# Optimization experiments

Measured on AMD Instinct MI355X. Metric: run time of the kernel, lower is better.

The kernel has to match this reference:

```python
import jax, jax.numpy as jnp
import numpy as np

N_TOKENS = 16384
DIM = 4096
NUM_EXPERTS = 128
TOP_K = 8


def setup_inputs() -> dict:
    key = jax.random.key(0)
    k1, k2 = jax.random.split(key)
    x = jax.random.normal(k1, (N_TOKENS, DIM), dtype=jnp.float32)
    gate_w = jax.random.normal(k2, (NUM_EXPERTS, DIM), dtype=jnp.float32) * (DIM ** -0.5)
    return {"x": x, "gate_w": gate_w, "experts_per_token": TOP_K, "num_experts": NUM_EXPERTS}


def reference(x, gate_w, experts_per_token, num_experts):
    # gate: x @ W^T -> (N, E) logits
    scores = jnp.einsum('nd,ed->ne', x, gate_w)
    # softmax in fp32, cast back to input dtype
    probs = jax.nn.softmax(scores.astype(jnp.float32), axis=-1).astype(x.dtype)
    # stable descending argsort (argsort of negated probs, stable)
    sorted_indices = jnp.argsort(-probs, axis=1, stable=True)
    selected_experts = sorted_indices[:, :experts_per_token]            # (N, k)
    top_scores = jnp.take_along_axis(probs, selected_experts, axis=1)   # (N, k)
    # norm_topk_prob=True: renormalize selected weights to sum to 1
    denom = jnp.clip(top_scores.sum(axis=-1, keepdims=True), 1e-8, None)
    top_scores = top_scores / denom
    flat_experts = selected_experts.reshape(-1)                         # (N*k,)
    num_tokens_per_expert = jnp.bincount(flat_experts, length=num_experts)
    # stable sort token-slots by expert id for expert grouping
    perm = jnp.argsort(flat_experts, stable=True)                       # (N*k,)
    top_scores_sorted = top_scores.reshape(-1)[perm]
    token_indices = perm // experts_per_token
    return top_scores_sorted, token_indices, num_tokens_per_expert
```

## Files before the change

### kernel.cpp

```cpp
#include <hip/hip_runtime.h>
#include <math.h>

typedef _Float16 f16;
typedef f16 f16x8 __attribute__((ext_vector_type(8)));
typedef float f32x4 __attribute__((ext_vector_type(4)));

#define NT    16384
#define DIM   4096
#define NEXP  128
#define TOPK  8
#define NFLAT (NT * TOPK)
#define BT    32
#define NBLK  (NT / BT)
#define BK    64
#define NSTEP (DIM / BK)

#define COUNTS_OFF 0
#define SEL_OFF    1024
#define WGT_OFF    (SEL_OFF + NFLAT * 4)
#define BH_OFF     (WGT_OFF + NFLAT * 4)
#define BO_OFF     (BH_OFF + NEXP * NBLK * 4)
#define WPK_OFF    (BO_OFF + NEXP * NBLK * 4)

#define G1P __attribute__((address_space(1)))
#define L3P __attribute__((address_space(3)))

__device__ __forceinline__ void gload_lds16(const void* g, void* l) {
    __builtin_amdgcn_global_load_lds((const G1P unsigned int*)g,
                                     (L3P unsigned int*)l, 16, 0, 0);
}

__device__ __forceinline__ void split2(float v, f16& h, f16& m) {
    h = (f16)v;
    m = (f16)((v - (float)h) * 2048.0f);
}

__global__ __launch_bounds__(256)
void wsplit_kernel(const float* __restrict__ gw, char* __restrict__ wpk) {
    const int t = blockIdx.x * 256 + threadIdx.x;
    const int l = t & 63, kkc = (t >> 6) & 1, w = (t >> 7) & 7, st = t >> 10;
    const int e = w * 16 + (l & 15);
    const int k0 = st * 64 + kkc * 32 + (l >> 4) * 8;
    float4 a = *(const float4*)&gw[e * 4096 + k0];
    float4 b = *(const float4*)&gw[e * 4096 + k0 + 4];
    union { f16 f[8]; uint4 u; } ph, pm;
    split2(a.x * 64.f, ph.f[0], pm.f[0]); split2(a.y * 64.f, ph.f[1], pm.f[1]);
    split2(a.z * 64.f, ph.f[2], pm.f[2]); split2(a.w * 64.f, ph.f[3], pm.f[3]);
    split2(b.x * 64.f, ph.f[4], pm.f[4]); split2(b.y * 64.f, ph.f[5], pm.f[5]);
    split2(b.z * 64.f, ph.f[6], pm.f[6]); split2(b.w * 64.f, ph.f[7], pm.f[7]);
    const size_t base = ((size_t)(st * 8 + w) * 4 + kkc) * 1024 + l * 16;
    *(uint4*)(wpk + base)        = ph.u;
    *(uint4*)(wpk + base + 2048) = pm.u;
}

__global__ __launch_bounds__(512, 4)
void fused_kernel(const float* __restrict__ x, const char* __restrict__ wpk,
                  float* __restrict__ wgt, int* __restrict__ sel,
                  int* __restrict__ counts, int* __restrict__ bh) {
    __shared__ __align__(16) char smem[81920];
    char* WB = smem + 16384;

    const int tid  = threadIdx.x;
    const int tok0 = blockIdx.x * BT;
    const int lane = tid & 63, w = tid >> 6;
    const int fr = lane & 15, hi = lane >> 4;
    const int srow = tid >> 4;
    const int skq  = (tid & 15) * 4;
    const int xi = srow >> 4, xfr = srow & 15;
    const int xkk = skq >> 5, xhi = (skq >> 3) & 3, xo = skq & 7;
    const int slot = xhi * 16 + xfr;
    const int xwb = ((xi * 2 + xkk) * 64 + (slot ^ (xhi << 1))) * 16 + xo * 2;
    const int lxs = (lane ^ ((lane >> 4) << 1)) * 16;

    f32x4 acc0[2], acc1[2];
#pragma unroll
    for (int i = 0; i < 2; ++i) {
        acc0[i] = (f32x4){0.f, 0.f, 0.f, 0.f};
        acc1[i] = (f32x4){0.f, 0.f, 0.f, 0.f};
    }

    const size_t xrow = (size_t)(tok0 + srow) * DIM;

#define X_PREF(RA, SI) RA = *(const float4*)&x[xrow + (size_t)(SI) * BK + skq];
#define W_PREF(SI, B) { \
    const char* wsrc = wpk + ((size_t)(SI) * 8 + w) * 4096 + lane * 16; \
    char* wdst = WB + (B) * 32768 + w * 4096; \
    gload_lds16(wsrc,        wdst); \
    gload_lds16(wsrc + 1024, wdst + 1024); \
    gload_lds16(wsrc + 2048, wdst + 2048); \
    gload_lds16(wsrc + 3072, wdst + 3072); }
#define STAGE(CUR, RA) { \
    union { f16 f[4]; uint2 u; } ph, pm; \
    split2(RA.x, ph.f[0], pm.f[0]); split2(RA.y, ph.f[1], pm.f[1]); \
    split2(RA.z, ph.f[2], pm.f[2]); split2(RA.w, ph.f[3], pm.f[3]); \
    *(uint2*)(smem + (CUR) * 4096 + xwb) = ph.u; \
    *(uint2*)(smem + 8192 + (CUR) * 4096 + xwb) = pm.u; }
#define COMPUTE(CUR) { \
    _Pragma("unroll") \
    for (int kk = 0; kk < 2; ++kk) { \
        f16x8 ah[2], am[2]; \
        _Pragma("unroll") \
        for (int i = 0; i < 2; ++i) { \
            const int xb = (CUR) * 4096 + (i * 2 + kk) * 1024 + lxs; \
            ah[i] = *(const f16x8*)(smem + xb); \
            am[i] = *(const f16x8*)(smem + 8192 + xb); \
        } \
        const int wb = (CUR) * 32768 + w * 4096 + kk * 1024 + lane * 16; \
        f16x8 bhf = *(const f16x8*)(WB + wb); \
        f16x8 bmf = *(const f16x8*)(WB + wb + 2048); \
        _Pragma("unroll") \
        for (int i = 0; i < 2; ++i) { \
            acc0[i] = __builtin_amdgcn_mfma_f32_16x16x32_f16(ah[i], bhf, acc0[i], 0, 0, 0); \
            acc1[i] = __builtin_amdgcn_mfma_f32_16x16x32_f16(ah[i], bmf, acc1[i], 0, 0, 0); \
            acc1[i] = __builtin_amdgcn_mfma_f32_16x16x32_f16(am[i], bhf, acc1[i], 0, 0, 0); \
        } \
    } }
#define STEP(CUR, RA, PX, PW, SI, VMSTR) { \
    STAGE(CUR, RA); \
    asm volatile("s_waitcnt lgkmcnt(0)" ::: "memory"); \
    __builtin_amdgcn_s_barrier(); \
    if (PX) { X_PREF(RA, (SI) + 2); } \
    if (PW) { W_PREF((SI) + 1, (CUR) ^ 1); } \
    asm volatile("s_waitcnt vmcnt(" VMSTR ")" ::: "memory"); \
    __builtin_amdgcn_sched_barrier(0); \
    __builtin_amdgcn_s_setprio(1); \
    COMPUTE(CUR); \
    __builtin_amdgcn_s_setprio(0); }

    float4 ra0, ra1;
    X_PREF(ra0, 0);
    X_PREF(ra1, 1);
    W_PREF(0, 0);

    for (int st = 0; st < 62; st += 2) {
        STEP(0, ra0, 1, 1, st, "5");
        STEP(1, ra1, 1, 1, st + 1, "5");
    }
    STEP(0, ra0, 0, 1, 62, "4");
    STEP(1, ra1, 0, 0, 63, "0");

    __syncthreads();

    float* S = (float*)smem;
    int*   h = (int*)(smem + 18432);
#pragma unroll
    for (int i = 0; i < 2; ++i)
#pragma unroll
        for (int q = 0; q < 4; ++q) {
            int t = i * 16 + hi * 4 + q;
            int e = w * 16 + fr;
            S[t * 132 + e] = (acc0[i][q] + acc1[i][q] * (1.0f / 2048.0f)) * (1.0f / 64.0f);
        }
    if (tid < NEXP) h[tid] = 0;
    __syncthreads();

    if (tid < BT) {
        float bs[8]; int bi[8];
#pragma unroll
        for (int r = 0; r < 8; ++r) { bs[r] = -3.0e38f; bi[r] = 0; }
        for (int e = 0; e < NEXP; ++e) {
            float s = S[tid * 132 + e];
            if (s > bs[7]) {
                int pos = 7;
#pragma unroll
                for (int q = 6; q >= 0; q--) pos = (s > bs[q]) ? q : pos;
#pragma unroll
                for (int q = 7; q >= 1; q--) {
                    bool sh = (q > pos);
                    bs[q] = sh ? bs[q - 1] : bs[q];
                    bi[q] = sh ? bi[q - 1] : bi[q];
                }
#pragma unroll
                for (int q = 0; q < 8; q++)
                    if (q == pos) { bs[q] = s; bi[q] = e; }
            }
        }
        float m = bs[0], sum = 0.f, ex[8];
#pragma unroll
        for (int r = 0; r < 8; ++r) { ex[r] = expf(bs[r] - m); sum += ex[r]; }
        float inv = 1.f / fmaxf(sum, 1e-8f);
        const int tok = tok0 + tid;
#pragma unroll
        for (int r = 0; r < 8; ++r) {
            wgt[tok * TOPK + r] = ex[r] * inv;
            sel[tok * TOPK + r] = bi[r];
            atomicAdd(&h[bi[r]], 1);
        }
    }
    __syncthreads();
    if (tid < NEXP) {
        int c = h[tid];
        bh[tid * NBLK + blockIdx.x] = c;
        if (c) atomicAdd(&counts[tid], c);
    }
}

__global__ void scan_kernel(const int* __restrict__ bh, const int* __restrict__ counts,
                            int* __restrict__ bo, float* __restrict__ out) {
    const int e = blockIdx.x, tid = threadIdx.x;
    __shared__ int pre[NEXP];
    __shared__ int wsum[8];
    if (tid < NEXP) pre[tid] = counts[tid];
    __syncthreads();
#pragma unroll
    for (int d = 1; d < NEXP; d <<= 1) {
        int o = (tid < NEXP && tid >= d) ? pre[tid - d] : 0;
        __syncthreads();
        if (tid < NEXP) pre[tid] += o;
        __syncthreads();
    }
    const int gb = (e == 0) ? 0 : pre[e - 1];
    if (tid == 0) out[2 * NFLAT + e] = (float)counts[e];

    const int lane = tid & 63, wid = tid >> 6;
    int v = bh[e * NBLK + tid];
    int sc = v;
#pragma unroll
    for (int d = 1; d < 64; d <<= 1) {
        int o = __shfl_up(sc, d);
        sc += (lane >= d) ? o : 0;
    }
    if (lane == 63) wsum[wid] = sc;
    __syncthreads();
    int add = 0;
#pragma unroll
    for (int ww = 0; ww < 8; ww++) add += (ww < wid) ? wsum[ww] : 0;
    bo[e * NBLK + tid] = gb + sc - v + add;
}

__global__ void scatter_kernel(const int* __restrict__ sel, const float* __restrict__ wgt,
                               const int* __restrict__ bo, float* __restrict__ out) {
    const int tid = threadIdx.x, b = blockIdx.x;
    const int i = b * 256 + tid;
    const int e = sel[i];
    const int lane = tid & 63, wid = tid >> 6;
    unsigned long long m = ~0ull;
#pragma unroll
    for (int bit = 0; bit < 7; bit++) {
        unsigned long long bal = __ballot((e >> bit) & 1);
        m &= ((e >> bit) & 1) ? bal : ~bal;
    }
    unsigned long long lower = (lane == 0) ? 0ull : (~0ull >> (64 - lane));
    int wrank = __popcll(m & lower);

    __shared__ int wh_[4][NEXP];
    ((int*)wh_)[tid] = 0; ((int*)wh_)[tid + 256] = 0;
    __syncthreads();
    if (wrank == 0) wh_[wid][e] = __popcll(m);
    __syncthreads();
    int off = 0;
#pragma unroll
    for (int ww = 0; ww < 4; ww++) off += (ww < wid) ? wh_[ww][e] : 0;

    int pos = bo[e * NBLK + b] + off + wrank;
    out[pos] = wgt[i];
    out[NFLAT + pos] = (float)(i >> 3);
}

extern "C" void kernel_launch(void* const* d_in, const int* in_sizes, int n_in,
                              void* d_out, int out_size, void* d_ws, size_t ws_size,
                              hipStream_t stream) {
    const float* x  = (const float*)d_in[0];
    const float* gw = (const float*)d_in[1];
    float* out = (float*)d_out;
    char*  ws  = (char*)d_ws;

    int*   counts = (int*)(ws + COUNTS_OFF);
    int*   sel    = (int*)(ws + SEL_OFF);
    float* wgt    = (float*)(ws + WGT_OFF);
    int*   bh     = (int*)(ws + BH_OFF);
    int*   bo     = (int*)(ws + BO_OFF);
    char*  wpk    = ws + WPK_OFF;

    hipMemsetAsync(counts, 0, NEXP * sizeof(int), stream);

    wsplit_kernel<<<256, 256, 0, stream>>>(gw, wpk);
    fused_kernel<<<NBLK, 512, 0, stream>>>(x, wpk, wgt, sel, counts, bh);
    scan_kernel<<<NEXP, 512, 0, stream>>>(bh, counts, bo, out);
    scatter_kernel<<<NBLK, 256, 0, stream>>>(sel, wgt, bo, out);
}
```

Measured before the change: 127.9 us.

## Double token tile to 64 with 2x2 per-warp MFMA register blocking

The token tile per block grows from 32 to 64, and each warp now computes a 2x2 grid of 16x16 output tiles, so every expert-weight fragment loaded into LDS is reused across twice as many tokens. This roughly halves the L2 traffic spent re-reading the packed gate weights. X prefetch now uses two float4 loads per thread, and the wait and barrier ordering is reworked so the weight prefetch is issued before the X prefetch. In exchange, LDS per block rises to 96KB and the occupancy hint drops to 2, which likely allows only one block per CU. The per-expert histogram is split into two 32-token halves so the scan and scatter kernels keep their 512-block layout.

```diff
diff --git a/kernel.cpp b/kernel.cpp
--- a/kernel.cpp
+++ b/kernel.cpp
@@ -10,8 +10,9 @@
 #define NEXP  128
 #define TOPK  8
 #define NFLAT (NT * TOPK)
-#define BT    32
-#define NBLK  (NT / BT)
+#define BT    64
+#define NFB   (NT / BT)
+#define SBLK  512
 #define BK    64
 #define NSTEP (DIM / BK)
 
@@ -19,8 +20,8 @@
 #define SEL_OFF    1024
 #define WGT_OFF    (SEL_OFF + NFLAT * 4)
 #define BH_OFF     (WGT_OFF + NFLAT * 4)
-#define BO_OFF     (BH_OFF + NEXP * NBLK * 4)
-#define WPK_OFF    (BO_OFF + NEXP * NBLK * 4)
+#define BO_OFF     (BH_OFF + NEXP * SBLK * 4)
+#define WPK_OFF    (BO_OFF + NEXP * SBLK * 4)
 
 #define G1P __attribute__((address_space(1)))
 #define L3P __attribute__((address_space(3)))
@@ -38,8 +39,8 @@
 __global__ __launch_bounds__(256)
 void wsplit_kernel(const float* __restrict__ gw, char* __restrict__ wpk) {
     const int t = blockIdx.x * 256 + threadIdx.x;
-    const int l = t & 63, kkc = (t >> 6) & 1, w = (t >> 7) & 7, st = t >> 10;
-    const int e = w * 16 + (l & 15);
+    const int l = t & 63, kkc = (t >> 6) & 1, g = (t >> 7) & 7, st = t >> 10;
+    const int e = g * 16 + (l & 15);
     const int k0 = st * 64 + kkc * 32 + (l >> 4) * 8;
     float4 a = *(const float4*)&gw[e * 4096 + k0];
     float4 b = *(const float4*)&gw[e * 4096 + k0 + 4];
@@ -48,118 +49,133 @@
     split2(a.z * 64.f, ph.f[2], pm.f[2]); split2(a.w * 64.f, ph.f[3], pm.f[3]);
     split2(b.x * 64.f, ph.f[4], pm.f[4]); split2(b.y * 64.f, ph.f[5], pm.f[5]);
     split2(b.z * 64.f, ph.f[6], pm.f[6]); split2(b.w * 64.f, ph.f[7], pm.f[7]);
-    const size_t base = ((size_t)(st * 8 + w) * 4 + kkc) * 1024 + l * 16;
+    const size_t base = ((size_t)(st * 8 + g) * 4 + kkc) * 1024 + l * 16;
     *(uint4*)(wpk + base)        = ph.u;
     *(uint4*)(wpk + base + 2048) = pm.u;
 }
 
-__global__ __launch_bounds__(512, 4)
+__global__ __launch_bounds__(512, 2)
 void fused_kernel(const float* __restrict__ x, const char* __restrict__ wpk,
                   float* __restrict__ wgt, int* __restrict__ sel,
                   int* __restrict__ counts, int* __restrict__ bh) {
-    __shared__ __align__(16) char smem[81920];
-    char* WB = smem + 16384;
+    __shared__ __align__(16) char smem[98304];
+    char* WB = smem + 32768;
 
     const int tid  = threadIdx.x;
     const int tok0 = blockIdx.x * BT;
-    const int lane = tid & 63, w = tid >> 6;
+    const int lane = tid & 63, wid = tid >> 6;
+    const int r = wid >> 2, eg = wid & 3;
     const int fr = lane & 15, hi = lane >> 4;
-    const int srow = tid >> 4;
-    const int skq  = (tid & 15) * 4;
+    const int srow = tid >> 3;
+    const int skq  = (tid & 7) * 8;
     const int xi = srow >> 4, xfr = srow & 15;
-    const int xkk = skq >> 5, xhi = (skq >> 3) & 3, xo = skq & 7;
-    const int slot = xhi * 16 + xfr;
-    const int xwb = ((xi * 2 + xkk) * 64 + (slot ^ (xhi << 1))) * 16 + xo * 2;
+    const int xkk = skq >> 5, xhi = (skq >> 3) & 3;
+    const int xslot = xhi * 16 + xfr;
+    const int xwb = ((xi * 2 + xkk) * 64 + (xslot ^ ((xslot >> 4) << 1))) * 16;
     const int lxs = (lane ^ ((lane >> 4) << 1)) * 16;
-
-    f32x4 acc0[2], acc1[2];
-#pragma unroll
-    for (int i = 0; i < 2; ++i) {
-        acc0[i] = (f32x4){0.f, 0.f, 0.f, 0.f};
-        acc1[i] = (f32x4){0.f, 0.f, 0.f, 0.f};
-    }
+    const int myg = 2 * eg + r;
+
+    f32x4 acc0[2][2], acc1[2][2];
+#pragma unroll
+    for (int i = 0; i < 2; ++i)
+#pragma unroll
+        for (int j = 0; j < 2; ++j) {
+            acc0[i][j] = (f32x4){0.f, 0.f, 0.f, 0.f};
+            acc1[i][j] = (f32x4){0.f, 0.f, 0.f, 0.f};
+        }
 
     const size_t xrow = (size_t)(tok0 + srow) * DIM;
 
-#define X_PREF(RA, SI) RA = *(const float4*)&x[xrow + (size_t)(SI) * BK + skq];
+#define X_PREF(RA, RB, SI) { \
+    RA = *(const float4*)&x[xrow + (size_t)(SI) * BK + skq]; \
+    RB = *(const float4*)&x[xrow + (size_t)(SI) * BK + skq + 4]; }
 #define W_PREF(SI, B) { \
-    const char* wsrc = wpk + ((size_t)(SI) * 8 + w) * 4096 + lane * 16; \
-    char* wdst = WB + (B) * 32768 + w * 4096; \
+    const char* wsrc = wpk + ((size_t)(SI) * 8 + myg) * 4096 + lane * 16; \
+    char* wdst = WB + (B) * 32768 + myg * 4096; \
     gload_lds16(wsrc,        wdst); \
     gload_lds16(wsrc + 1024, wdst + 1024); \
     gload_lds16(wsrc + 2048, wdst + 2048); \
     gload_lds16(wsrc + 3072, wdst + 3072); }
-#define STAGE(CUR, RA) { \
-    union { f16 f[4]; uint2 u; } ph, pm; \
+#define STAGE(CUR, RA, RB) { \
+    union { f16 f[8]; f16x8 v; } ph, pm; \
     split2(RA.x, ph.f[0], pm.f[0]); split2(RA.y, ph.f[1], pm.f[1]); \
     split2(RA.z, ph.f[2], pm.f[2]); split2(RA.w, ph.f[3], pm.f[3]); \
-    *(uint2*)(smem + (CUR) * 4096 + xwb) = ph.u; \
-    *(uint2*)(smem + 8192 + (CUR) * 4096 + xwb) = pm.u; }
+    split2(RB.x, ph.f[4], pm.f[4]); split2(RB.y, ph.f[5], pm.f[5]); \
+    split2(RB.z, ph.f[6], pm.f[6]); split2(RB.w, ph.f[7], pm.f[7]); \
+    *(f16x8*)(smem + (CUR) * 8192 + xwb) = ph.v; \
+    *(f16x8*)(smem + 16384 + (CUR) * 8192 + xwb) = pm.v; }
 #define COMPUTE(CUR) { \
     _Pragma("unroll") \
     for (int kk = 0; kk < 2; ++kk) { \
-        f16x8 ah[2], am[2]; \
+        f16x8 ah[2], am[2], bhf[2], bmf[2]; \
         _Pragma("unroll") \
         for (int i = 0; i < 2; ++i) { \
-            const int xb = (CUR) * 4096 + (i * 2 + kk) * 1024 + lxs; \
+            const int xb = (CUR) * 8192 + ((2 * r + i) * 2 + kk) * 1024 + lxs; \
             ah[i] = *(const f16x8*)(smem + xb); \
-            am[i] = *(const f16x8*)(smem + 8192 + xb); \
+            am[i] = *(const f16x8*)(smem + 16384 + xb); \
         } \
-        const int wb = (CUR) * 32768 + w * 4096 + kk * 1024 + lane * 16; \
-        f16x8 bhf = *(const f16x8*)(WB + wb); \
-        f16x8 bmf = *(const f16x8*)(WB + wb + 2048); \
-        _Pragma("unroll") \
-        for (int i = 0; i < 2; ++i) { \
-            acc0[i] = __builtin_amdgcn_mfma_f32_16x16x32_f16(ah[i], bhf, acc0[i], 0, 0, 0); \
-            acc1[i] = __builtin_amdgcn_mfma_f32_16x16x32_f16(ah[i], bmf, acc1[i], 0, 0, 0); \
-            acc1[i] = __builtin_amdgcn_mfma_f32_16x16x32_f16(am[i], bhf, acc1[i], 0, 0, 0); \
+        _Pragma("unroll") \
+        for (int j = 0; j < 2; ++j) { \
+            const int wb = (CUR) * 32768 + (2 * eg + j) * 4096 + kk * 1024 + lane * 16; \
+            bhf[j] = *(const f16x8*)(WB + wb); \
+            bmf[j] = *(const f16x8*)(WB + wb + 2048); \
+        } \
+        _Pragma("unroll") \
+        for (int i = 0; i < 2; ++i) \
+        _Pragma("unroll") \
+        for (int j = 0; j < 2; ++j) { \
+            acc0[i][j] = __builtin_amdgcn_mfma_f32_16x16x32_f16(ah[i], bhf[j], acc0[i][j], 0, 0, 0); \
+            acc1[i][j] = __builtin_amdgcn_mfma_f32_16x16x32_f16(ah[i], bmf[j], acc1[i][j], 0, 0, 0); \
+            acc1[i][j] = __builtin_amdgcn_mfma_f32_16x16x32_f16(am[i], bhf[j], acc1[i][j], 0, 0, 0); \
         } \
     } }
-#define STEP(CUR, RA, PX, PW, SI, VMSTR) { \
-    STAGE(CUR, RA); \
-    asm volatile("s_waitcnt lgkmcnt(0)" ::: "memory"); \
+#define STEP(CUR, RA, RB, PX, PW, SI, VMSTR) { \
+    STAGE(CUR, RA, RB); \
+    asm volatile("s_waitcnt lgkmcnt(0) vmcnt(" VMSTR ")" ::: "memory"); \
     __builtin_amdgcn_s_barrier(); \
-    if (PX) { X_PREF(RA, (SI) + 2); } \
     if (PW) { W_PREF((SI) + 1, (CUR) ^ 1); } \
-    asm volatile("s_waitcnt vmcnt(" VMSTR ")" ::: "memory"); \
     __builtin_amdgcn_sched_barrier(0); \
+    if (PX) { X_PREF(RA, RB, (SI) + 2); } \
     __builtin_amdgcn_s_setprio(1); \
     COMPUTE(CUR); \
     __builtin_amdgcn_s_setprio(0); }
 
-    float4 ra0, ra1;
-    X_PREF(ra0, 0);
-    X_PREF(ra1, 1);
+    float4 a0, b0, a1, b1;
     W_PREF(0, 0);
+    X_PREF(a0, b0, 0);
+    X_PREF(a1, b1, 1);
 
     for (int st = 0; st < 62; st += 2) {
-        STEP(0, ra0, 1, 1, st, "5");
-        STEP(1, ra1, 1, 1, st + 1, "5");
-    }
-    STEP(0, ra0, 0, 1, 62, "4");
-    STEP(1, ra1, 0, 0, 63, "0");
-
-    __syncthreads();
-
-    float* S = (float*)smem;
-    int*   h = (int*)(smem + 18432);
+        STEP(0, a0, b0, 1, 1, st, "2");
+        STEP(1, a1, b1, 1, 1, st + 1, "2");
+    }
+    STEP(0, a0, b0, 0, 1, 62, "2");
+    STEP(1, a1, b1, 0, 0, 63, "0");
+
+    __syncthreads();
+
+    float* S  = (float*)smem;
+    int*   h2 = (int*)(smem + 34816);
 #pragma unroll
     for (int i = 0; i < 2; ++i)
 #pragma unroll
-        for (int q = 0; q < 4; ++q) {
-            int t = i * 16 + hi * 4 + q;
-            int e = w * 16 + fr;
-            S[t * 132 + e] = (acc0[i][q] + acc1[i][q] * (1.0f / 2048.0f)) * (1.0f / 64.0f);
-        }
-    if (tid < NEXP) h[tid] = 0;
+        for (int j = 0; j < 2; ++j)
+#pragma unroll
+            for (int q = 0; q < 4; ++q) {
+                int t = r * 32 + i * 16 + hi * 4 + q;
+                int e = eg * 32 + j * 16 + fr;
+                S[t * 129 + e] =
+                    (acc0[i][j][q] + acc1[i][j][q] * (1.0f / 2048.0f)) * (1.0f / 64.0f);
+            }
+    if (tid < 256) h2[tid] = 0;
     __syncthreads();
 
     if (tid < BT) {
         float bs[8]; int bi[8];
 #pragma unroll
-        for (int r = 0; r < 8; ++r) { bs[r] = -3.0e38f; bi[r] = 0; }
+        for (int q = 0; q < 8; ++q) { bs[q] = -3.0e38f; bi[q] = 0; }
         for (int e = 0; e < NEXP; ++e) {
-            float s = S[tid * 132 + e];
+            float s = S[tid * 129 + e];
             if (s > bs[7]) {
                 int pos = 7;
 #pragma unroll
@@ -177,21 +193,22 @@
         }
         float m = bs[0], sum = 0.f, ex[8];
 #pragma unroll
-        for (int r = 0; r < 8; ++r) { ex[r] = expf(bs[r] - m); sum += ex[r]; }
+        for (int q = 0; q < 8; ++q) { ex[q] = expf(bs[q] - m); sum += ex[q]; }
         float inv = 1.f / fmaxf(sum, 1e-8f);
         const int tok = tok0 + tid;
 #pragma unroll
-        for (int r = 0; r < 8; ++r) {
-            wgt[tok * TOPK + r] = ex[r] * inv;
-            sel[tok * TOPK + r] = bi[r];
-            atomicAdd(&h[bi[r]], 1);
+        for (int q = 0; q < 8; ++q) {
+            wgt[tok * TOPK + q] = ex[q] * inv;
+            sel[tok * TOPK + q] = bi[q];
+            atomicAdd(&h2[(tid >> 5) * NEXP + bi[q]], 1);
         }
     }
     __syncthreads();
     if (tid < NEXP) {
-        int c = h[tid];
-        bh[tid * NBLK + blockIdx.x] = c;
-        if (c) atomicAdd(&counts[tid], c);
+        int c0 = h2[tid], c1 = h2[NEXP + tid];
+        bh[tid * SBLK + 2 * blockIdx.x]     = c0;
+        bh[tid * SBLK + 2 * blockIdx.x + 1] = c1;
+        if (c0 + c1) atomicAdd(&counts[tid], c0 + c1);
     }
 }
 
@@ -213,7 +230,7 @@
     if (tid == 0) out[2 * NFLAT + e] = (float)counts[e];
 
     const int lane = tid & 63, wid = tid >> 6;
-    int v = bh[e * NBLK + tid];
+    int v = bh[e * SBLK + tid];
     int sc = v;
 #pragma unroll
     for (int d = 1; d < 64; d <<= 1) {
@@ -225,7 +242,7 @@
     int add = 0;
 #pragma unroll
     for (int ww = 0; ww < 8; ww++) add += (ww < wid) ? wsum[ww] : 0;
-    bo[e * NBLK + tid] = gb + sc - v + add;
+    bo[e * SBLK + tid] = gb + sc - v + add;
 }
 
 __global__ void scatter_kernel(const int* __restrict__ sel, const float* __restrict__ wgt,
@@ -252,7 +269,7 @@
 #pragma unroll
     for (int ww = 0; ww < 4; ww++) off += (ww < wid) ? wh_[ww][e] : 0;
 
-    int pos = bo[e * NBLK + b] + off + wrank;
+    int pos = bo[e * SBLK + b] + off + wrank;
     out[pos] = wgt[i];
     out[NFLAT + pos] = (float)(i >> 3);
 }
@@ -275,7 +292,7 @@
     hipMemsetAsync(counts, 0, NEXP * sizeof(int), stream);
 
     wsplit_kernel<<<256, 256, 0, stream>>>(gw, wpk);
-    fused_kernel<<<NBLK, 512, 0, stream>>>(x, wpk, wgt, sel, counts, bh);
+    fused_kernel<<<NFB, 512, 0, stream>>>(x, wpk, wgt, sel, counts, bh);
     scan_kernel<<<NEXP, 512, 0, stream>>>(bh, counts, bo, out);
-    scatter_kernel<<<NBLK, 256, 0, stream>>>(sel, wgt, bo, out);
-}
+    scatter_kernel<<<SBLK, 256, 0, stream>>>(sel, wgt, bo, out);
+}
```

Measured after the change: 118.0 us. 7.7% less time.
